# Optimization experiments

Measured on AMD Instinct MI355X. Metric: run time of the kernel, lower is better.

The kernel has to match this reference:

```python
import jax, jax.numpy as jnp
import numpy as np

# (row/col slice start, slice end, index offset added to final argmax) per part e
SPECS = [(5, 201, 5), (5, 201, 5), (5, 103, 5), (54, 152, 54), (103, 201, 103)]


def _build_part_att(x, e):
    """x: [L, b, N, N] stacked per-layer attention maps.
    Returns [L, b, M, M] where M = 1 + (hi-lo): token e + its part window,
    sliced on both the row and column dims (faithful to the torch cats)."""
    lo, hi, _ = SPECS[e]
    rows = jnp.concatenate([x[:, :, e:e + 1, :], x[:, :, lo:hi, :]], axis=2)
    att = jnp.concatenate([rows[:, :, :, e:e + 1], rows[:, :, :, lo:hi]], axis=3)
    return att


def setup_inputs() -> dict:
    key = jax.random.key(0)
    # 12 layers, batch 128, 201 tokens (5 part tokens + 196 patches)
    x = jax.random.normal(key, (12, 128, 201, 201), dtype=jnp.float32)
    return {"x": x}


def reference(x):
    max_p, max_inx = [], []
    for e in range(5):  # fixed small structural loop over the 5 parts
        att = _build_part_att(x, e)  # [L, b, M, M]
        # attention rollout: last = att[L-1] @ ... @ att[1] @ att[0]
        def step(carry, a):
            return jnp.matmul(a, carry), None
        last, _ = jax.lax.scan(step, att[0], att[1:])
        row = last[:, 0, 1:]  # [b, M-1] : attention of token e onto its patches
        max_p.append(jnp.max(row, axis=-1, keepdims=True))
        max_inx.append(jnp.argmax(row, axis=-1, keepdims=True) + SPECS[e][2])
    return jnp.stack(max_p, axis=0), jnp.stack(max_inx, axis=0).astype(jnp.int32)
```

## Files before the change

kernel.cpp:

```cpp
#include <hip/hip_runtime.h>

#define NB 128
#define NTOK 201
#define EW 210

__device__ __forceinline__ void lds_barrier() {
    asm volatile("s_waitcnt lgkmcnt(0)" ::: "memory");
    __builtin_amdgcn_s_barrier();
}

template<int M>
__device__ __forceinline__ void chain4(
    const float* __restrict__ xb, float* __restrict__ out,
    const int e, const int b, const int lo,
    float* u, float (*part)[212], float* rv, int* rix)
{
    constexpr int W4 = (M + 5) / 4;
    constexpr int NK = (M + 3) / 4;

    const int tid = threadIdx.x;
    const int g   = tid & 63;
    const int w   = tid >> 6;

    const size_t plane = (size_t)NTOK * NTOK;
    const float* L11 = xb + (size_t)(11 * NB) * plane + (size_t)e * NTOK;

    const int trg = (b + 2 * lo - 1 + w) & 3;
    const int C   = lo - trg;
    const int sel = (b + lo - 1 + w + e) & 3;
    const int col0 = (g < W4) ? (C + 4 * g) : (e - sel);

    if (tid < 212) u[tid] = 0.f;
    __syncthreads();
    if (tid >= 3 && tid < M + 2) u[tid] = L11[lo - 3 + tid];
    if (tid == EW)               u[tid] = L11[e];
    __syncthreads();

    const size_t rstep = (size_t)(4 * NTOK);
    const float* A = xb + (size_t)(10 * NB) * plane;

    for (int l = 10; l >= 0; --l) {
        if (g <= W4) {
            float4 acc = make_float4(0.f, 0.f, 0.f, 0.f);
            float shead = 0.f;
            if (w == 0) {
                const float hw = u[EW];
                if (g < W4) {
                    const float* hp = A + (size_t)e * NTOK + col0;
                    acc.x = hw * hp[0]; acc.y = hw * hp[1];
                    acc.z = hw * hp[2]; acc.w = hw * hp[3];
                } else {
                    shead = hw * A[(size_t)e * NTOK + e];
                }
            }
            const float* rp = A + (size_t)(lo - 1 + w) * NTOK + col0;
            #pragma unroll
            for (int k = 0; k < NK - 1; ++k) {
                const float wt = u[w + 2 + 4 * k];
                const float4 a = *(const float4*)(rp + rstep * k);
                acc.x += wt * a.x; acc.y += wt * a.y;
                acc.z += wt * a.z; acc.w += wt * a.w;
            }
            {
                constexpr int k = NK - 1;
                const int r = w + 4 * k;
                const float wt = u[r + 2];
                const float4 a = *(const float4*)(rp + rstep * k
                                                  - ((r >= M) ? rstep : 0));
                acc.x += wt * a.x; acc.y += wt * a.y;
                acc.z += wt * a.z; acc.w += wt * a.w;
            }
            if (g < W4) {
                *(float4*)&part[w][4 * g] = acc;
            } else {
                const float se = (sel == 0) ? acc.x :
                                 (sel == 1) ? acc.y :
                                 (sel == 2) ? acc.z : acc.w;
                part[w][EW] = se + shead;
            }
        }
        lds_barrier();
        if (tid >= 3 && tid < M + 2) {
            float s = 0.f;
            #pragma unroll
            for (int q = 0; q < 4; ++q) {
                const int tq = (b + 2 * lo - 1 + q) & 3;
                s += part[q][tid - 3 + tq];
            }
            u[tid] = s;
        } else if (tid == EW) {
            u[EW] = part[0][EW] + part[1][EW] + part[2][EW] + part[3][EW];
        }
        lds_barrier();
        A -= (size_t)NB * plane;
    }

    {
        float v = -INFINITY; int idx = 0x7fffffff;
        if (tid >= 3 && tid < M + 2) { v = u[tid]; idx = tid; }
        rv[tid] = v; rix[tid] = idx;
    }
    __syncthreads();
    for (int s = 128; s > 0; s >>= 1) {
        if (tid < s) {
            const float v2 = rv[tid + s]; const int i2 = rix[tid + s];
            if (v2 > rv[tid] || (v2 == rv[tid] && i2 < rix[tid])) {
                rv[tid] = v2; rix[tid] = i2;
            }
        }
        __syncthreads();
    }
    if (tid == 0) {
        out[e * NB + b]       = rv[0];
        out[640 + e * NB + b] = (float)(lo - 3 + rix[0]);
    }
}

__global__ __launch_bounds__(256, 4) void part_att_kernel(
    const float* __restrict__ x, float* __restrict__ out)
{
    __shared__ float u[212];
    __shared__ float part[4][212];
    __shared__ float rv[256];
    __shared__ int   rix[256];

    const int bid = blockIdx.x;
    const int e   = bid >> 7;
    const int b   = bid & 127;
    const float* xb = x + (size_t)b * ((size_t)NTOK * NTOK);

    if (e < 2) {
        chain4<197>(xb, out, e, b, 5, u, part, rv, rix);
    } else {
        const int lo = (e == 2) ? 5 : (e == 3) ? 54 : 103;
        chain4<99>(xb, out, e, b, lo, u, part, rv, rix);
    }
}

extern "C" void kernel_launch(void* const* d_in, const int* in_sizes, int n_in,
                              void* d_out, int out_size, void* d_ws, size_t ws_size,
                              hipStream_t stream) {
    (void)in_sizes; (void)n_in; (void)d_ws; (void)ws_size; (void)out_size;
    const float* x = (const float*)d_in[0];
    float* out = (float*)d_out;
    part_att_kernel<<<dim3(640), dim3(256), 0, stream>>>(x, out);
}
```

Baseline: 46.33 us.

## Replicate rollout vector per wave and double-buffer partials to drop a barrier

Each wavefront now keeps its own copy of the rollout vector `u` and recomputes the 4-way partial-sum reduction redundantly, instead of one shared copy written by a subset of threads. The `part` buffer is double-buffered across layer iterations, which makes the second block-wide barrier per layer unnecessary. This is meant to cut synchronisation latency in the serial 11-step chain. In exchange it does four times the reduction work and LDS writes per step and uses more shared memory, which could affect occupancy.

```diff
diff --git a/kernel.cpp b/kernel.cpp
--- a/kernel.cpp
+++ b/kernel.cpp
@@ -13,7 +13,7 @@
 __device__ __forceinline__ void chain4(
     const float* __restrict__ xb, float* __restrict__ out,
     const int e, const int b, const int lo,
-    float* u, float (*part)[212], float* rv, int* rix)
+    float (*u4)[212], float (*part)[4][212], float* rv, int* rix)
 {
     constexpr int W4 = (M + 5) / 4;
     constexpr int NK = (M + 3) / 4;
@@ -30,21 +30,30 @@
     const int sel = (b + lo - 1 + w + e) & 3;
     const int col0 = (g < W4) ? (C + 4 * g) : (e - sel);
 
-    if (tid < 212) u[tid] = 0.f;
-    __syncthreads();
-    if (tid >= 3 && tid < M + 2) u[tid] = L11[lo - 3 + tid];
-    if (tid == EW)               u[tid] = L11[e];
+    float* uw = u4[w];
+
+    #pragma unroll
+    for (int k2 = 0; k2 < 4; ++k2) {
+        const int s = g + 64 * k2;
+        if (s < 212) {
+            float v = 0.f;
+            if (s >= 3 && s < M + 2) v = L11[lo - 3 + s];
+            if (s == EW)             v = L11[e];
+            uw[s] = v;
+        }
+    }
     __syncthreads();
 
     const size_t rstep = (size_t)(4 * NTOK);
     const float* A = xb + (size_t)(10 * NB) * plane;
+    int pb = 0;
 
     for (int l = 10; l >= 0; --l) {
         if (g <= W4) {
             float4 acc = make_float4(0.f, 0.f, 0.f, 0.f);
             float shead = 0.f;
             if (w == 0) {
-                const float hw = u[EW];
+                const float hw = uw[EW];
                 if (g < W4) {
                     const float* hp = A + (size_t)e * NTOK + col0;
                     acc.x = hw * hp[0]; acc.y = hw * hp[1];
@@ -56,7 +65,7 @@
             const float* rp = A + (size_t)(lo - 1 + w) * NTOK + col0;
             #pragma unroll
             for (int k = 0; k < NK - 1; ++k) {
-                const float wt = u[w + 2 + 4 * k];
+                const float wt = uw[w + 2 + 4 * k];
                 const float4 a = *(const float4*)(rp + rstep * k);
                 acc.x += wt * a.x; acc.y += wt * a.y;
                 acc.z += wt * a.z; acc.w += wt * a.w;
@@ -64,40 +73,45 @@
             {
                 constexpr int k = NK - 1;
                 const int r = w + 4 * k;
-                const float wt = u[r + 2];
+                const float wt = uw[r + 2];
                 const float4 a = *(const float4*)(rp + rstep * k
                                                   - ((r >= M) ? rstep : 0));
                 acc.x += wt * a.x; acc.y += wt * a.y;
                 acc.z += wt * a.z; acc.w += wt * a.w;
             }
             if (g < W4) {
-                *(float4*)&part[w][4 * g] = acc;
+                *(float4*)&part[pb][w][4 * g] = acc;
             } else {
                 const float se = (sel == 0) ? acc.x :
                                  (sel == 1) ? acc.y :
                                  (sel == 2) ? acc.z : acc.w;
-                part[w][EW] = se + shead;
+                part[pb][w][EW] = se + shead;
             }
         }
         lds_barrier();
-        if (tid >= 3 && tid < M + 2) {
-            float s = 0.f;
-            #pragma unroll
-            for (int q = 0; q < 4; ++q) {
-                const int tq = (b + 2 * lo - 1 + q) & 3;
-                s += part[q][tid - 3 + tq];
+        #pragma unroll
+        for (int k2 = 0; k2 < 4; ++k2) {
+            const int p = 3 + g + 64 * k2;
+            if (p < M + 2) {
+                float s = 0.f;
+                #pragma unroll
+                for (int q = 0; q < 4; ++q) {
+                    const int tq = (b + 2 * lo - 1 + q) & 3;
+                    s += part[pb][q][p - 3 + tq];
+                }
+                uw[p] = s;
+            } else if (p == EW) {
+                uw[EW] = part[pb][0][EW] + part[pb][1][EW]
+                       + part[pb][2][EW] + part[pb][3][EW];
             }
-            u[tid] = s;
-        } else if (tid == EW) {
-            u[EW] = part[0][EW] + part[1][EW] + part[2][EW] + part[3][EW];
         }
-        lds_barrier();
+        pb ^= 1;
         A -= (size_t)NB * plane;
     }
 
     {
         float v = -INFINITY; int idx = 0x7fffffff;
-        if (tid >= 3 && tid < M + 2) { v = u[tid]; idx = tid; }
+        if (tid >= 3 && tid < M + 2) { v = uw[tid]; idx = tid; }
         rv[tid] = v; rix[tid] = idx;
     }
     __syncthreads();
@@ -119,8 +133,8 @@
 __global__ __launch_bounds__(256, 4) void part_att_kernel(
     const float* __restrict__ x, float* __restrict__ out)
 {
-    __shared__ float u[212];
-    __shared__ float part[4][212];
+    __shared__ float u4[4][212];
+    __shared__ float part[2][4][212];
     __shared__ float rv[256];
     __shared__ int   rix[256];
 
@@ -130,10 +144,10 @@
     const float* xb = x + (size_t)b * ((size_t)NTOK * NTOK);
 
     if (e < 2) {
-        chain4<197>(xb, out, e, b, 5, u, part, rv, rix);
+        chain4<197>(xb, out, e, b, 5, u4, part, rv, rix);
     } else {
         const int lo = (e == 2) ? 5 : (e == 3) ? 54 : 103;
-        chain4<99>(xb, out, e, b, lo, u, part, rv, rix);
+        chain4<99>(xb, out, e, b, lo, u4, part, rv, rix);
     }
 }
 
```

After: 45.87 us, median of 3. No clear change (-1.0%).
